# Kernel optimization log

Measured on AMD Instinct MI355X. Metric: run time of the kernel, lower is better.

The kernel has to match this reference:

```python
import jax, jax.numpy as jnp
import numpy as np

H = 128  # hidden size
F_IN = 33  # GRU input size
STEPS = 64


def setup_inputs() -> dict:
    key = jax.random.key(0)
    ks = jax.random.split(key, 10)
    x = jax.random.normal(ks[0], (STEPS, 17), dtype=jnp.float32)
    ip = jax.random.randint(ks[1], (STEPS, 8), 0, 256)
    port = jax.random.randint(ks[2], (STEPS, 2), 0, 70000)
    hidden = jnp.zeros((1, 1, H), dtype=jnp.float32)
    # learned parameters (torch default init ~ U(-1/sqrt(H), 1/sqrt(H)) for GRU, N(0,1) for embeddings)
    s = 1.0 / np.sqrt(H)
    ip_emb = jax.random.normal(ks[3], (256, 1), dtype=jnp.float32)
    port_emb = jax.random.normal(ks[4], (70000, 4), dtype=jnp.float32)
    W_ih = jax.random.uniform(ks[5], (3 * H, F_IN), minval=-s, maxval=s, dtype=jnp.float32)
    W_hh = jax.random.uniform(ks[6], (3 * H, H), minval=-s, maxval=s, dtype=jnp.float32)
    b_ih = jax.random.uniform(ks[7], (3 * H,), minval=-s, maxval=s, dtype=jnp.float32)
    b_hh = jax.random.uniform(ks[8], (3 * H,), minval=-s, maxval=s, dtype=jnp.float32)
    return {"x": x, "ip": ip, "port": port, "hidden": hidden,
            "ip_emb": ip_emb, "port_emb": port_emb,
            "W_ih": W_ih, "W_hh": W_hh, "b_ih": b_ih, "b_hh": b_hh}


def reference(x, ip, port, hidden, ip_emb, port_emb, W_ih, W_hh, b_ih, b_hh):
    # Embedding lookups + flatten: [64, 8*1] and [64, 2*4]
    ipf = ip_emb[ip].reshape(STEPS, -1)
    pf = port_emb[port].reshape(STEPS, -1)
    xi = jnp.concatenate([x, ipf, pf], axis=1)  # [64, 33]
    h0 = hidden[0, 0]  # [128]; same initial hidden reused at every step in the original loop
    # Single batched GRU cell over all 64 "steps" (they are independent given shared h0)
    gi = xi @ W_ih.T + b_ih          # [64, 3H]
    gh = h0 @ W_hh.T + b_hh          # [3H], broadcast over the 64 rows
    i_r, i_z, i_n = jnp.split(gi, 3, axis=1)
    h_r, h_z, h_n = jnp.split(gh, 3)
    r = jax.nn.sigmoid(i_r + h_r)
    z = jax.nn.sigmoid(i_z + h_z)
    n = jnp.tanh(i_n + r * h_n)
    outputs = (1.0 - z) * n + z * h0  # [64, 128]
    new_hidden = outputs[STEPS - 1].reshape(1, 1, H)  # self.hidden after last iteration
    return outputs, new_hidden
```

## Files before the change

### kernel.cpp

```cpp
#include <hip/hip_runtime.h>
#include <hip/hip_bf16.h>

#define H 128
#define STEPS 64
#define F_IN 33
#define R3H 384

__global__ __launch_bounds__(256) void gh_kernel(
    const float* __restrict__ hidden,
    const float* __restrict__ W_hh,
    const float* __restrict__ b_hh,
    float* __restrict__ gh)
{
    const int wave = threadIdx.x >> 6;
    const int lane = threadIdx.x & 63;
    const int row  = blockIdx.x * 4 + wave;
    const float* wrow = W_hh + (size_t)row * H;
    float p = wrow[lane] * hidden[lane] + wrow[lane + 64] * hidden[lane + 64];
    #pragma unroll
    for (int m = 32; m >= 1; m >>= 1) p += __shfl_xor(p, m, 64);
    if (lane == 0) gh[row] = p + b_hh[row];
}

__global__ __launch_bounds__(128) void Encoder_57380763074770_kernel(
    const float* __restrict__ x,
    const int*   __restrict__ ip,
    const int*   __restrict__ port,
    const float* __restrict__ hidden,
    const float* __restrict__ ip_emb,
    const float* __restrict__ port_emb,
    const float* __restrict__ W_ih,
    const float* __restrict__ b_ih,
    const float* __restrict__ gh,
    float* __restrict__ out)
{
    __shared__ float xi[F_IN];
    __shared__ float h0s[H];
    __shared__ float wih[R3H * F_IN];

    const int s   = blockIdx.x;
    const int tid = threadIdx.x;

    if (tid < 17) {
        xi[tid] = x[s * 17 + tid];
    } else if (tid < 25) {
        xi[tid] = ip_emb[ip[s * 8 + (tid - 17)]];
    } else if (tid < F_IN) {
        int c = tid - 25;
        xi[tid] = port_emb[port[s * 2 + (c >> 2)] * 4 + (c & 3)];
    }
    h0s[tid] = hidden[tid];

    {
        const float4* w4 = (const float4*)W_ih;
        float4*       l4 = (float4*)wih;
        #pragma unroll
        for (int i = 0; i < (R3H * F_IN) / 4 / 128 + 1; ++i) {
            int idx = tid + i * 128;
            if (idx < (R3H * F_IN) / 4) l4[idx] = w4[idx];
        }
    }

    const int j = tid;
    const float ghr = gh[j];
    const float ghz = gh[j + H];
    const float ghn = gh[j + 2 * H];
    float gir = b_ih[j];
    float giz = b_ih[j + H];
    float gin = b_ih[j + 2 * H];

    __syncthreads();

    const float* vr = wih + j * F_IN;
    const float* vz = wih + (j + H) * F_IN;
    const float* vn = wih + (j + 2 * H) * F_IN;
    #pragma unroll
    for (int k = 0; k < F_IN; ++k) {
        const float xv = xi[k];
        gir = fmaf(xv, vr[k], gir);
        giz = fmaf(xv, vz[k], giz);
        gin = fmaf(xv, vn[k], gin);
    }

    const float r = 1.0f / (1.0f + __expf(-(gir + ghr)));
    const float z = 1.0f / (1.0f + __expf(-(giz + ghz)));
    float a = gin + r * ghn;
    a = fminf(fmaxf(a, -15.0f), 15.0f);
    const float e2 = __expf(2.0f * a);
    const float n = (e2 - 1.0f) / (e2 + 1.0f);
    const float o = (1.0f - z) * n + z * h0s[j];

    out[s * H + j] = o;
    if (s == STEPS - 1) out[STEPS * H + j] = o;
}

extern "C" void kernel_launch(void* const* d_in, const int* in_sizes, int n_in,
                              void* d_out, int out_size, void* d_ws, size_t ws_size,
                              hipStream_t stream) {
    const float* x        = (const float*)d_in[0];
    const int*   ip       = (const int*)  d_in[1];
    const int*   port     = (const int*)  d_in[2];
    const float* hidden   = (const float*)d_in[3];
    const float* ip_emb   = (const float*)d_in[4];
    const float* port_emb = (const float*)d_in[5];
    const float* W_ih     = (const float*)d_in[6];
    const float* W_hh     = (const float*)d_in[7];
    const float* b_ih     = (const float*)d_in[8];
    const float* b_hh     = (const float*)d_in[9];
    float* out = (float*)d_out;
    float* gh  = (float*)d_ws;

    gh_kernel<<<96, 256, 0, stream>>>(hidden, W_hh, b_hh, gh);
    Encoder_57380763074770_kernel<<<STEPS, H, 0, stream>>>(
        x, ip, port, hidden, ip_emb, port_emb, W_ih, b_ih, gh, out);
}
```

Baseline: 77.13 us.

## Fuse hidden-gate matvec into main GRU kernel, dropping separate gh launch

Drops the separate gh_kernel launch. Every block now computes W_hh·h0 itself, staging W_hh into LDS in four 96-row chunks with an XOR swizzle to avoid bank conflicts, then reuses the same buffer for W_ih. The goal is to remove one kernel launch and the dependency through global memory. The cost is that all 64 blocks redundantly read the 196KB W_hh and each block adds several barriers and serial LDS passes.

Measured after the change: 82.27 us. +6.7%, slower.

```diff
diff --git a/kernel.cpp b/kernel.cpp
--- a/kernel.cpp
+++ b/kernel.cpp
@@ -5,22 +5,6 @@
 #define STEPS 64
 #define F_IN 33
 #define R3H 384
-
-__global__ __launch_bounds__(256) void gh_kernel(
-    const float* __restrict__ hidden,
-    const float* __restrict__ W_hh,
-    const float* __restrict__ b_hh,
-    float* __restrict__ gh)
-{
-    const int wave = threadIdx.x >> 6;
-    const int lane = threadIdx.x & 63;
-    const int row  = blockIdx.x * 4 + wave;
-    const float* wrow = W_hh + (size_t)row * H;
-    float p = wrow[lane] * hidden[lane] + wrow[lane + 64] * hidden[lane + 64];
-    #pragma unroll
-    for (int m = 32; m >= 1; m >>= 1) p += __shfl_xor(p, m, 64);
-    if (lane == 0) gh[row] = p + b_hh[row];
-}
 
 __global__ __launch_bounds__(128) void Encoder_57380763074770_kernel(
     const float* __restrict__ x,
@@ -30,16 +14,18 @@
     const float* __restrict__ ip_emb,
     const float* __restrict__ port_emb,
     const float* __restrict__ W_ih,
+    const float* __restrict__ W_hh,
     const float* __restrict__ b_ih,
-    const float* __restrict__ gh,
+    const float* __restrict__ b_hh,
     float* __restrict__ out)
 {
-    __shared__ float xi[F_IN];
-    __shared__ float h0s[H];
-    __shared__ float wih[R3H * F_IN];
+    __shared__ float4 buf[3168];
+    __shared__ float4 h0v[32];
+    __shared__ float  xi[F_IN + 3];
 
+    const int tid = threadIdx.x;
     const int s   = blockIdx.x;
-    const int tid = threadIdx.x;
+    const int j   = tid;
 
     if (tid < 17) {
         xi[tid] = x[s * 17 + tid];
@@ -49,31 +35,59 @@
         int c = tid - 25;
         xi[tid] = port_emb[port[s * 2 + (c >> 2)] * 4 + (c & 3)];
     }
-    h0s[tid] = hidden[tid];
+    if (tid < 32) h0v[tid] = ((const float4*)hidden)[tid];
 
-    {
-        const float4* w4 = (const float4*)W_ih;
-        float4*       l4 = (float4*)wih;
+    float ghv0 = 0.f, ghv1 = 0.f, ghv2 = 0.f;
+    const float4* whh4 = (const float4*)W_hh;
+
+    for (int c = 0; c < 4; ++c) {
         #pragma unroll
-        for (int i = 0; i < (R3H * F_IN) / 4 / 128 + 1; ++i) {
-            int idx = tid + i * 128;
-            if (idx < (R3H * F_IN) / 4) l4[idx] = w4[idx];
+        for (int it = 0; it < 24; ++it) {
+            const int g = tid + (it << 7);
+            const int r = g >> 5;
+            const int m = g & 31;
+            buf[r * 32 + (m ^ (r & 31))] = whh4[c * 3072 + g];
         }
+        __syncthreads();
+
+        const int lo = c * 96;
+        #pragma unroll
+        for (int t = 0; t < 3; ++t) {
+            const int lr = j + (t << 7) - lo;
+            if (lr >= 0 && lr < 96) {
+                const float4* trow = buf + lr * 32;
+                const int key = lr & 31;
+                float a = 0.f;
+                #pragma unroll 8
+                for (int i = 0; i < 32; ++i) {
+                    const float4 w = trow[i ^ key];
+                    const float4 h = h0v[i];
+                    a = fmaf(w.x, h.x, fmaf(w.y, h.y,
+                        fmaf(w.z, h.z, fmaf(w.w, h.w, a))));
+                }
+                if (t == 0) ghv0 = a;
+                else if (t == 1) ghv1 = a;
+                else ghv2 = a;
+            }
+        }
+        __syncthreads();
     }
 
-    const int j = tid;
-    const float ghr = gh[j];
-    const float ghz = gh[j + H];
-    const float ghn = gh[j + 2 * H];
+    const float4* wi4 = (const float4*)W_ih;
+    #pragma unroll
+    for (int it = 0; it < 25; ++it) {
+        const int idx = tid + (it << 7);
+        if (idx < 3168) buf[idx] = wi4[idx];
+    }
+    __syncthreads();
+
+    const float* wihf = (const float*)buf;
     float gir = b_ih[j];
     float giz = b_ih[j + H];
     float gin = b_ih[j + 2 * H];
-
-    __syncthreads();
-
-    const float* vr = wih + j * F_IN;
-    const float* vz = wih + (j + H) * F_IN;
-    const float* vn = wih + (j + 2 * H) * F_IN;
+    const float* vr = wihf + j * F_IN;
+    const float* vz = wihf + (j + H) * F_IN;
+    const float* vn = wihf + (j + 2 * H) * F_IN;
     #pragma unroll
     for (int k = 0; k < F_IN; ++k) {
         const float xv = xi[k];
@@ -82,13 +96,18 @@
         gin = fmaf(xv, vn[k], gin);
     }
 
+    const float ghr = ghv0 + b_hh[j];
+    const float ghz = ghv1 + b_hh[j + H];
+    const float ghn = ghv2 + b_hh[j + 2 * H];
+
     const float r = 1.0f / (1.0f + __expf(-(gir + ghr)));
     const float z = 1.0f / (1.0f + __expf(-(giz + ghz)));
     float a = gin + r * ghn;
     a = fminf(fmaxf(a, -15.0f), 15.0f);
     const float e2 = __expf(2.0f * a);
     const float n = (e2 - 1.0f) / (e2 + 1.0f);
-    const float o = (1.0f - z) * n + z * h0s[j];
+    const float h0j = ((const float*)h0v)[j];
+    const float o = (1.0f - z) * n + z * h0j;
 
     out[s * H + j] = o;
     if (s == STEPS - 1) out[STEPS * H + j] = o;
@@ -108,9 +127,7 @@
     const float* b_ih     = (const float*)d_in[8];
     const float* b_hh     = (const float*)d_in[9];
     float* out = (float*)d_out;
-    float* gh  = (float*)d_ws;
 
-    gh_kernel<<<96, 256, 0, stream>>>(hidden, W_hh, b_hh, gh);
     Encoder_57380763074770_kernel<<<STEPS, H, 0, stream>>>(
-        x, ip, port, hidden, ip_emb, port_emb, W_ih, b_ih, gh, out);
+        x, ip, port, hidden, ip_emb, port_emb, W_ih, W_hh, b_ih, b_hh, out);
 }
```
